# Performance work log

Measured on AMD Instinct MI355X. Metric: run time of the kernel, lower is better.

Reference implementation:

```python
import jax, jax.numpy as jnp
import numpy as np

VOCAB = 8192
K = 3  # order_k


def setup_inputs() -> dict:
    key = jax.random.key(0)
    kx, kp = jax.random.split(key)
    x = jax.random.randint(kx, (8, 2048), 0, VOCAB)
    params = jax.random.normal(kp, (K, K), dtype=jnp.float32) * 0.02
    return {"x": x, "params": params}


def _get_windows(x):
    # windows[b, t, i, :] = one_hot(x[b, t - i]) (zeros for t - i < 0)
    B, T = x.shape
    emb = jax.nn.one_hot(x, VOCAB, dtype=jnp.float32)          # (B, T, V)
    pad = jnp.zeros((B, K - 1, VOCAB), dtype=jnp.float32)
    padded = jnp.concatenate([pad, emb], axis=1)               # (B, T+K-1, V)
    # small fixed loop over K offsets; stack -> (B, T, K, V)
    return jnp.stack([padded[:, K - 1 - i:K - 1 - i + T, :] for i in range(K)], axis=2)


def reference(x, params):
    B, T = x.shape
    windows = _get_windows(x)                                  # (B, T, K, V)
    q_window = windows[:, -1, :, :]                            # (B, K, V)
    # mask_first=False -> k_windows = windows
    match = jnp.einsum('biv,btjv->btij', q_window, windows)    # (B, T, K, K)
    scores = jnp.einsum('btij,ij->bt', match, params)          # (B, T)
    scores = scores.at[:, -1].set(-1e9)                        # mask last position
    attn = jax.nn.softmax(scores, axis=-1)                     # (B, T)
    values = windows[:, :, 0, :]                               # (B, T, V)
    return jnp.einsum('bt,btv->bv', attn, values)              # (B, V)
```

## Files before the change

### kernel.cpp

```cpp
#include <hip/hip_runtime.h>


constexpr int T = 2048;
constexpr int V = 8192;
constexpr int BLOCK = 256;
constexpr int PER = T / BLOCK;
constexpr int NWAVE = BLOCK / 64;

__global__ __launch_bounds__(BLOCK)
void ca_kernel(const int* __restrict__ x, const float* __restrict__ params,
               float* __restrict__ out) {
    const int b = blockIdx.x;
    const int tid = threadIdx.x;

    __shared__ int   s_x[T];
    __shared__ float s_acc[V];
    __shared__ float s_red[NWAVE];

    {
        const int4* xb4 = reinterpret_cast<const int4*>(x + b * T);
        int4* sx4 = reinterpret_cast<int4*>(s_x);
        #pragma unroll
        for (int k = 0; k < (T / 4) / BLOCK; ++k)
            sx4[tid + k * BLOCK] = xb4[tid + k * BLOCK];

        float4* sa4 = reinterpret_cast<float4*>(s_acc);
        const float4 z = make_float4(0.f, 0.f, 0.f, 0.f);
        #pragma unroll
        for (int k = 0; k < (V / 4) / BLOCK; ++k)
            sa4[tid + k * BLOCK] = z;
    }

    const float p00 = params[0], p01 = params[1], p02 = params[2];
    const float p10 = params[3], p11 = params[4], p12 = params[5];
    const float p20 = params[6], p21 = params[7], p22 = params[8];

    __syncthreads();
    const int q0 = s_x[T - 1], q1 = s_x[T - 2], q2 = s_x[T - 3];

    float e[PER];
    float lsum = 0.f;
    #pragma unroll
    for (int k = 0; k < PER; ++k) {
        const int t = tid + k * BLOCK;
        float s = 0.f;
        const int t0 = s_x[t];
        if (t0 == q0) s += p00;
        if (t0 == q1) s += p10;
        if (t0 == q2) s += p20;
        if (t >= 1) {
            const int t1 = s_x[t - 1];
            if (t1 == q0) s += p01;
            if (t1 == q1) s += p11;
            if (t1 == q2) s += p21;
        }
        if (t >= 2) {
            const int t2 = s_x[t - 2];
            if (t2 == q0) s += p02;
            if (t2 == q1) s += p12;
            if (t2 == q2) s += p22;
        }
        if (t == T - 1) s = -1.0e9f;
        e[k] = expf(s);
        lsum += e[k];
    }

    #pragma unroll
    for (int off = 32; off >= 1; off >>= 1)
        lsum += __shfl_down(lsum, off, 64);
    const int wave = tid >> 6, lane = tid & 63;
    if (lane == 0) s_red[wave] = lsum;
    __syncthreads();
    float S = 0.f;
    #pragma unroll
    for (int w = 0; w < NWAVE; ++w) S += s_red[w];
    const float inv = 1.f / S;

    #pragma unroll
    for (int k = 0; k < PER; ++k) {
        const int t = tid + k * BLOCK;
        atomicAdd(&s_acc[s_x[t]], e[k] * inv);
    }
    __syncthreads();

    float4* ob4 = reinterpret_cast<float4*>(out + b * V);
    const float4* sa4 = reinterpret_cast<const float4*>(s_acc);
    #pragma unroll
    for (int k = 0; k < (V / 4) / BLOCK; ++k)
        ob4[tid + k * BLOCK] = sa4[tid + k * BLOCK];
}

extern "C" void kernel_launch(void* const* d_in, const int* in_sizes, int n_in,
                              void* d_out, int out_size, void* d_ws, size_t ws_size,
                              hipStream_t stream) {
    const int* x = (const int*)d_in[0];
    const float* params = (const float*)d_in[1];
    float* out = (float*)d_out;
    const int B = in_sizes[0] / T;
    ca_kernel<<<B, BLOCK, 0, stream>>>(x, params, out);
}
```

Measured before the change: 58.79 us.

## Split vocab across 8 blocks per batch and load tokens directly into registers

Launches 8 blocks per batch row, each owning one eighth of the vocabulary, so the grid grows from 8 to 64 blocks and more CUs take part. Every block recomputes the full softmax over T from tokens read straight from global memory into registers (contiguous 8 per thread, plus two halo tokens). The shared x buffer and its barrier are gone. Each block scatters only the tokens that fall in its chunk, and the zero-fill and output copy shrink to one chunk. The cost is softmax work repeated eight times per row.

```diff
diff --git a/kernel.cpp b/kernel.cpp
--- a/kernel.cpp
+++ b/kernel.cpp
@@ -6,61 +6,63 @@
 constexpr int BLOCK = 256;
 constexpr int PER = T / BLOCK;
 constexpr int NWAVE = BLOCK / 64;
+constexpr int NCHUNK = 8;
+constexpr int CHUNK = V / NCHUNK;
 
 __global__ __launch_bounds__(BLOCK)
 void ca_kernel(const int* __restrict__ x, const float* __restrict__ params,
                float* __restrict__ out) {
-    const int b = blockIdx.x;
+    const int b   = blockIdx.x >> 3;
+    const int c   = blockIdx.x & (NCHUNK - 1);
     const int tid = threadIdx.x;
 
-    __shared__ int   s_x[T];
-    __shared__ float s_acc[V];
+    __shared__ float s_acc[CHUNK];
     __shared__ float s_red[NWAVE];
 
-    {
-        const int4* xb4 = reinterpret_cast<const int4*>(x + b * T);
-        int4* sx4 = reinterpret_cast<int4*>(s_x);
-        #pragma unroll
-        for (int k = 0; k < (T / 4) / BLOCK; ++k)
-            sx4[tid + k * BLOCK] = xb4[tid + k * BLOCK];
+    reinterpret_cast<float4*>(s_acc)[tid] = make_float4(0.f, 0.f, 0.f, 0.f);
 
-        float4* sa4 = reinterpret_cast<float4*>(s_acc);
-        const float4 z = make_float4(0.f, 0.f, 0.f, 0.f);
-        #pragma unroll
-        for (int k = 0; k < (V / 4) / BLOCK; ++k)
-            sa4[tid + k * BLOCK] = z;
-    }
+    const int* xb = x + b * T;
+
+    const int q0 = xb[T - 1], q1 = xb[T - 2], q2 = xb[T - 3];
 
     const float p00 = params[0], p01 = params[1], p02 = params[2];
     const float p10 = params[3], p11 = params[4], p12 = params[5];
     const float p20 = params[6], p21 = params[7], p22 = params[8];
 
-    __syncthreads();
-    const int q0 = s_x[T - 1], q1 = s_x[T - 2], q2 = s_x[T - 3];
+    const int t0 = tid * PER;
+    int tok[PER];
+    int m2, m1;
+    {
+        const int4 a = *reinterpret_cast<const int4*>(xb + t0);
+        const int4 d = *reinterpret_cast<const int4*>(xb + t0 + 4);
+        tok[0] = a.x; tok[1] = a.y; tok[2] = a.z; tok[3] = a.w;
+        tok[4] = d.x; tok[5] = d.y; tok[6] = d.z; tok[7] = d.w;
+        if (tid > 0) {
+            const int2 p = *reinterpret_cast<const int2*>(xb + t0 - 2);
+            m2 = p.x; m1 = p.y;
+        } else {
+            m2 = -1; m1 = -1;
+        }
+    }
 
     float e[PER];
     float lsum = 0.f;
     #pragma unroll
     for (int k = 0; k < PER; ++k) {
-        const int t = tid + k * BLOCK;
+        const int tj0 = tok[k];
+        const int tj1 = (k >= 1) ? tok[k - 1] : m1;
+        const int tj2 = (k >= 2) ? tok[k - 2] : (k == 1 ? m1 : m2);
         float s = 0.f;
-        const int t0 = s_x[t];
-        if (t0 == q0) s += p00;
-        if (t0 == q1) s += p10;
-        if (t0 == q2) s += p20;
-        if (t >= 1) {
-            const int t1 = s_x[t - 1];
-            if (t1 == q0) s += p01;
-            if (t1 == q1) s += p11;
-            if (t1 == q2) s += p21;
-        }
-        if (t >= 2) {
-            const int t2 = s_x[t - 2];
-            if (t2 == q0) s += p02;
-            if (t2 == q1) s += p12;
-            if (t2 == q2) s += p22;
-        }
-        if (t == T - 1) s = -1.0e9f;
+        if (tj0 == q0) s += p00;
+        if (tj0 == q1) s += p10;
+        if (tj0 == q2) s += p20;
+        if (tj1 == q0) s += p01;
+        if (tj1 == q1) s += p11;
+        if (tj1 == q2) s += p21;
+        if (tj2 == q0) s += p02;
+        if (tj2 == q1) s += p12;
+        if (tj2 == q2) s += p22;
+        if (t0 + k == T - 1) s = -1.0e9f;
         e[k] = expf(s);
         lsum += e[k];
     }
@@ -76,18 +78,17 @@
     for (int w = 0; w < NWAVE; ++w) S += s_red[w];
     const float inv = 1.f / S;
 
+    const int vbase = c * CHUNK;
     #pragma unroll
     for (int k = 0; k < PER; ++k) {
-        const int t = tid + k * BLOCK;
-        atomicAdd(&s_acc[s_x[t]], e[k] * inv);
+        const int v = tok[k] - vbase;
+        if ((unsigned)v < (unsigned)CHUNK)
+            atomicAdd(&s_acc[v], e[k] * inv);
     }
     __syncthreads();
 
-    float4* ob4 = reinterpret_cast<float4*>(out + b * V);
-    const float4* sa4 = reinterpret_cast<const float4*>(s_acc);
-    #pragma unroll
-    for (int k = 0; k < (V / 4) / BLOCK; ++k)
-        ob4[tid + k * BLOCK] = sa4[tid + k * BLOCK];
+    reinterpret_cast<float4*>(out + b * V + vbase)[tid] =
+        reinterpret_cast<const float4*>(s_acc)[tid];
 }
 
 extern "C" void kernel_launch(void* const* d_in, const int* in_sizes, int n_in,
@@ -97,5 +98,5 @@
     const float* params = (const float*)d_in[1];
     float* out = (float*)d_out;
     const int B = in_sizes[0] / T;
-    ca_kernel<<<B, BLOCK, 0, stream>>>(x, params, out);
+    ca_kernel<<<B * NCHUNK, BLOCK, 0, stream>>>(x, params, out);
 }
```

Measured after the change: 55.70 us. -5.3%, faster.
